# Kernel tuning notes

Measured on AMD Instinct MI355X. Metric: run time of the kernel, lower is better.

Reference implementation:

```python
import jax, jax.numpy as jnp
import numpy as np

BETA = 0.95
THRESH = 1.0
T = 25
MAXD = 11      # dilated_kernel_size: 250//25=10 -> bumped to odd 11
LP = 10        # left_pad = 250//25
B = 1024
SIGINIT = 5.0  # max_delay // 2, SIG is frozen at this value


@jax.custom_vjp
def atan_spike(u):
    # heaviside forward, atan surrogate gradient (snntorch surrogate.atan, alpha=2)
    return (u > 0).astype(u.dtype)

def _atan_fwd(u):
    return atan_spike(u), u

def _atan_bwd(u, g):
    return (g / (1.0 + (jnp.pi * u) ** 2),)

atan_spike.defvjp(_atan_fwd, _atan_bwd)


def dcls_kernel(W, P, SIG):
    # DCLS 'gauss': gaussian-interpolated dense kernel.
    # W: (O, I, kc), P/SIG: (1, O, I, kc) -> dense kernel (O, I, MAXD)
    idx = jnp.arange(MAXD, dtype=W.dtype)
    Pc = P[0] + MAXD // 2                      # center positions in dense kernel
    S = jnp.abs(SIG[0]) + 0.27                 # sigma floor (DCLS epsilon)
    X = jnp.exp(-0.5 * ((idx[:, None, None, None] - Pc) / S) ** 2)  # (K,O,I,kc)
    X = X / (X.sum(axis=0, keepdims=True) + 1e-7)
    return jnp.einsum('oic,joic->oij', W, X)


def dcls_conv(x, W, P, SIG, b):
    # x: (B, C_in, L) -> (B, C_out, L - MAXD + 1), VALID conv like padding=0
    k = dcls_kernel(W, P, SIG)
    y = jax.lax.conv_general_dilated(x, k, (1,), 'VALID',
                                     dimension_numbers=('NCH', 'OIH', 'NCH'))
    return y + b[None, :, None]


def batchnorm(x, gamma, beta, mean, var, eps=1e-5):
    # eval-mode BatchNorm1d over (B, C, L)
    inv = gamma / jnp.sqrt(var + eps)
    return (x - mean[None, :, None]) * inv[None, :, None] + beta[None, :, None]


def lif_scan(x):
    # snntorch Leaky, reset_mechanism='subtract'; x: (B, C, T) input currents
    xT = jnp.moveaxis(x, 2, 0)  # (T, B, C)

    def step(mem, xt):
        reset = jax.lax.stop_gradient(atan_spike(mem - THRESH))  # detached reset
        mem = BETA * mem + xt - reset * THRESH
        spk = atan_spike(mem - THRESH)
        return mem, (spk, mem)

    _, (spk, mem) = jax.lax.scan(step, jnp.zeros_like(xT[0]), xT)
    return spk, mem  # each (T, B, C)


def pad_left(x):
    return jnp.pad(x, ((0, 0), (0, 0), (LP, 0)))


def setup_inputs() -> dict:
    key = jax.random.key(0)
    ks = jax.random.split(key, 16)

    def w_init(k, o, i):
        return jax.random.normal(k, (o, i, 1), jnp.float32) / np.sqrt(i)

    inp = {
        'data': jax.random.normal(ks[0], (B, T, 140), jnp.float32),
        'W1': w_init(ks[1], 256, 140),
        'b1': jax.random.normal(ks[2], (256,), jnp.float32) * 0.01,
        'P1': jax.random.uniform(ks[3], (1, 256, 140, 1), jnp.float32, -SIGINIT, SIGINIT),
        'SIG1': jnp.full((1, 256, 140, 1), SIGINIT, jnp.float32),
        'bn1_gamma': jax.random.uniform(ks[4], (256,), jnp.float32, 0.5, 1.5),
        'bn1_beta': jax.random.normal(ks[5], (256,), jnp.float32) * 0.1,
        'bn1_mean': jax.random.normal(ks[6], (256,), jnp.float32) * 0.1,
        'bn1_var': jax.random.uniform(ks[7], (256,), jnp.float32, 0.5, 1.5),
        'W2': w_init(ks[8], 256, 256),
        'b2': jax.random.normal(ks[9], (256,), jnp.float32) * 0.01,
        'P2': jax.random.uniform(ks[10], (1, 256, 256, 1), jnp.float32, -SIGINIT, SIGINIT),
        'SIG2': jnp.full((1, 256, 256, 1), SIGINIT, jnp.float32),
        'bn2_gamma': jax.random.uniform(ks[11], (256,), jnp.float32, 0.5, 1.5),
        'bn2_beta': jax.random.normal(ks[12], (256,), jnp.float32) * 0.1,
        'bn2_mean': jax.random.normal(ks[13], (256,), jnp.float32) * 0.1,
        'bn2_var': jax.random.uniform(ks[14], (256,), jnp.float32, 0.5, 1.5),
        'W3': w_init(ks[15], 20, 256),
        'b3': jnp.zeros((20,), jnp.float32),
        'P3': jax.random.uniform(jax.random.fold_in(key, 99), (1, 20, 256, 1), jnp.float32, -SIGINIT, SIGINIT),
        'SIG3': jnp.full((1, 20, 256, 1), SIGINIT, jnp.float32),
    }
    return inp


def reference(data, W1, b1, P1, SIG1, bn1_gamma, bn1_beta, bn1_mean, bn1_var,
              W2, b2, P2, SIG2, bn2_gamma, bn2_beta, bn2_mean, bn2_var,
              W3, b3, P3, SIG3):
    # data: (B, T, 140); pad time dim on the left, then to (B, C, L)
    x = jnp.moveaxis(jnp.pad(data, ((0, 0), (LP, 0), (0, 0))), 1, 2)  # (B,140,T+LP)
    x = batchnorm(dcls_conv(x, W1, P1, SIG1, b1), bn1_gamma, bn1_beta, bn1_mean, bn1_var)
    spk1, _ = lif_scan(x)                  # (T, B, 256)
    in1 = jnp.moveaxis(spk1, 0, 2)         # (B, 256, T)  (dropout eval = identity)

    x = batchnorm(dcls_conv(pad_left(in1), W2, P2, SIG2, b2),
                  bn2_gamma, bn2_beta, bn2_mean, bn2_var)
    spk2, _ = lif_scan(x)
    in2 = jnp.moveaxis(spk2, 0, 2)         # (B, 256, T)

    x = dcls_conv(pad_left(in2), W3, P3, SIG3, b3)  # (B, 20, T)
    spk3, mem3 = lif_scan(x)               # (T, B, 20) each
    return spk3, mem3
```

## Files before the change

kernel.cpp:

```cpp
#include <hip/hip_runtime.h>
#include <math.h>

#define BB 1024
#define TT 25
#define LP 10
#define MAXD 11

#define XR2 26
#define XC 264
#define XSZ2 (XR2 * XC)

#define IC1 140
#define ICP1 160
#define XC1 168
#define XSZ1 (XR2 * XC1)
#define SS1 (2 * XSZ1)

typedef __bf16 bf16x8 __attribute__((ext_vector_type(8)));
typedef float  f32x4  __attribute__((ext_vector_type(4)));

#define MFMA16(A, B, C) __builtin_amdgcn_mfma_f32_16x16x32_bf16((A), (B), (C), 0, 0, 0)

__global__ void gen_trip(const float* __restrict__ W,
                         const float* __restrict__ P,
                         const float* __restrict__ SIG,
                         __bf16* __restrict__ Khi, __bf16* __restrict__ Kmid,
                         __bf16* __restrict__ Klo,
                         int O, int Opad, int I, int Ipad) {
    int idx = blockIdx.x * blockDim.x + threadIdx.x;
    if (idx >= Opad * Ipad) return;
    int i = idx % Ipad;
    int o = idx / Ipad;
    if (o >= O || i >= I) {
#pragma unroll
        for (int j = 0; j < MAXD; ++j) {
            size_t ofs = ((size_t)(j * Opad + o)) * Ipad + i;
            Khi[ofs] = (__bf16)0.0f;
            Kmid[ofs] = (__bf16)0.0f;
            Klo[ofs] = (__bf16)0.0f;
        }
        return;
    }
    int widx = o * I + i;
    float w  = W[widx];
    float pc = P[widx] + (float)(MAXD / 2);
    float s  = fabsf(SIG[widx]) + 0.27f;
    float x[MAXD];
    float sum = 0.f;
#pragma unroll
    for (int j = 0; j < MAXD; ++j) {
        float d = ((float)j - pc) / s;
        x[j] = expf(-0.5f * d * d);
        sum += x[j];
    }
    float denom = sum + 1e-7f;
#pragma unroll
    for (int j = 0; j < MAXD; ++j) {
        float kv = w * (x[j] / denom);
        __bf16 h = (__bf16)kv;
        float  r1 = kv - (float)h;
        __bf16 m = (__bf16)r1;
        float  r2 = r1 - (float)m;
        __bf16 l = (__bf16)r2;
        size_t ofs = ((size_t)(j * Opad + o)) * Ipad + i;
        Khi[ofs] = h;
        Kmid[ofs] = m;
        Klo[ofs] = l;
    }
}

__global__ __launch_bounds__(512, 2)
void conv1_mfma(const float* __restrict__ xin,
                const __bf16* __restrict__ Khi,
                const __bf16* __restrict__ Kmid,
                const __bf16* __restrict__ Klo,
                const float* __restrict__ bias,
                const float* __restrict__ gamma,
                const float* __restrict__ beta,
                const float* __restrict__ mean,
                const float* __restrict__ var,
                __bf16* __restrict__ spk1) {
    __shared__ __align__(16) char smem[3 * SS1 * 2];
    __bf16* xs = (__bf16*)smem;
    float*  ys = (float*)smem;

    const int rr = blockIdx.x & 7;
    const int gg = blockIdx.x >> 3;
    const int pp = 2 * (rr + 8 * (gg >> 1)) + (gg & 1);
    const int b0 = pp * 2;

    const int tid  = threadIdx.x;
    const int w    = tid >> 6;
    const int lane = tid & 63;
    const int lm   = lane & 15;
    const int quad = lane >> 4;

    {
        uint32_t* xz = (uint32_t*)smem;
        for (int k = tid; k < 3 * SS1 / 2; k += 512) xz[k] = 0u;
    }
    __syncthreads();
#pragma unroll
    for (int bl = 0; bl < 2; ++bl) {
        const float* src = xin + (size_t)(b0 + bl) * (TT * IC1);
        for (int k = tid; k < TT * IC1; k += 512) {
            int t = k / IC1;
            int i = k - t * IC1;
            float x  = src[k];
            __bf16 h = (__bf16)x;
            float r1 = x - (float)h;
            __bf16 m = (__bf16)r1;
            float r2 = r1 - (float)m;
            __bf16 l = (__bf16)r2;
            int ofs = bl * XSZ1 + t * XC1 + i;
            xs[0 * SS1 + ofs] = h;
            xs[1 * SS1 + ofs] = m;
            xs[2 * SS1 + ofs] = l;
        }
    }
    __syncthreads();

    f32x4 acc[2][4];
#pragma unroll
    for (int p = 0; p < 2; ++p)
#pragma unroll
        for (int nt = 0; nt < 4; ++nt) acc[p][nt] = (f32x4){0.f, 0.f, 0.f, 0.f};

    auto loadA = [&](int n, bf16x8* Ah, bf16x8* Am, bf16x8* Al) {
        n = (n > 54) ? 54 : n;
        const int j = n / 5;
        const int ic = n - 5 * j;
        const size_t base =
            (size_t)(j * 256 + w * 32 + lm) * ICP1 + ic * 32 + quad * 8;
#pragma unroll
        for (int p = 0; p < 2; ++p) {
            Ah[p] = *(const bf16x8*)(Khi  + base + p * 16 * ICP1);
            Am[p] = *(const bf16x8*)(Kmid + base + p * 16 * ICP1);
            Al[p] = *(const bf16x8*)(Klo  + base + p * 16 * ICP1);
        }
    };

    auto step = [&](int n, bf16x8* Ah, bf16x8* Am, bf16x8* Al) {
        const int j = n / 5;
        const int ic = n - 5 * j;
        int r0 = lm + j - 10;          r0 = ((unsigned)r0 < 25u) ? r0 : 25;
        int r1 = 16 + lm + j - 10;     r1 = ((unsigned)r1 < 25u) ? r1 : 25;
        const int col = ic * 32 + quad * 8;
#pragma unroll
        for (int bl = 0; bl < 2; ++bl) {
            bf16x8 Bh[2], Bm[2], Bl[2];
#pragma unroll
            for (int th = 0; th < 2; ++th) {
                const int row = th ? r1 : r0;
                const int ofs = bl * XSZ1 + row * XC1 + col;
                Bh[th] = *(const bf16x8*)&xs[0 * SS1 + ofs];
                Bm[th] = *(const bf16x8*)&xs[1 * SS1 + ofs];
                Bl[th] = *(const bf16x8*)&xs[2 * SS1 + ofs];
            }
#pragma unroll
            for (int p = 0; p < 2; ++p)
#pragma unroll
                for (int th = 0; th < 2; ++th)
                    acc[p][bl * 2 + th] = MFMA16(Ah[p], Bh[th], acc[p][bl * 2 + th]);
#pragma unroll
            for (int p = 0; p < 2; ++p)
#pragma unroll
                for (int th = 0; th < 2; ++th)
                    acc[p][bl * 2 + th] = MFMA16(Ah[p], Bm[th], acc[p][bl * 2 + th]);
#pragma unroll
            for (int p = 0; p < 2; ++p)
#pragma unroll
                for (int th = 0; th < 2; ++th)
                    acc[p][bl * 2 + th] = MFMA16(Am[p], Bh[th], acc[p][bl * 2 + th]);
#pragma unroll
            for (int p = 0; p < 2; ++p)
#pragma unroll
                for (int th = 0; th < 2; ++th)
                    acc[p][bl * 2 + th] = MFMA16(Ah[p], Bl[th], acc[p][bl * 2 + th]);
#pragma unroll
            for (int p = 0; p < 2; ++p)
#pragma unroll
                for (int th = 0; th < 2; ++th)
                    acc[p][bl * 2 + th] = MFMA16(Am[p], Bm[th], acc[p][bl * 2 + th]);
#pragma unroll
            for (int p = 0; p < 2; ++p)
#pragma unroll
                for (int th = 0; th < 2; ++th)
                    acc[p][bl * 2 + th] = MFMA16(Al[p], Bh[th], acc[p][bl * 2 + th]);
        }
    };

    bf16x8 A0h[2], A0m[2], A0l[2], A1h[2], A1m[2], A1l[2];
    loadA(0, A0h, A0m, A0l);
    for (int n = 0; n < 54; n += 2) {
        loadA(n + 1, A1h, A1m, A1l);
        step(n, A0h, A0m, A0l);
        loadA(n + 2, A0h, A0m, A0l);
        step(n + 1, A1h, A1m, A1l);
    }
    step(54, A0h, A0m, A0l);

#pragma unroll
    for (int bl = 0; bl < 2; ++bl) {
        __syncthreads();
#pragma unroll
        for (int p = 0; p < 2; ++p)
#pragma unroll
            for (int th = 0; th < 2; ++th) {
                int t = th * 16 + lm;
                if (t < TT) {
                    int ob = w * 32 + p * 16 + quad * 4;
#pragma unroll
                    for (int v = 0; v < 4; ++v)
                        ys[(ob + v) * 27 + t] = acc[p][bl * 2 + th][v];
                }
            }
        __syncthreads();
        if (tid < 256) {
            const int o = tid;
            float scale = gamma[o] / sqrtf(var[o] + 1e-5f);
            float ofs   = (bias[o] - mean[o]) * scale + beta[o];
            unsigned short* dst =
                (unsigned short*)spk1 + (size_t)(b0 + bl) * (TT * 256) + o;
            const float* yrow = &ys[o * 27];
            float memv = 0.f;
#pragma unroll
            for (int t = 0; t < TT; ++t) {
                float a     = yrow[t] * scale + ofs;
                float reset = (memv > 1.0f) ? 1.0f : 0.f;
                memv        = 0.95f * memv + a - reset;
                dst[t * 256] = (memv > 1.0f) ? 0x3F80 : 0;
            }
        }
    }
}

__attribute__((amdgpu_waves_per_eu(4, 4)))
__global__ __launch_bounds__(512)
void conv2_mfma(const __bf16* __restrict__ spk1,
                const __bf16* __restrict__ Khi,
                const __bf16* __restrict__ Kmid,
                const __bf16* __restrict__ Klo,
                const float* __restrict__ bias,
                const float* __restrict__ gamma,
                const float* __restrict__ beta,
                const float* __restrict__ mean,
                const float* __restrict__ var,
                __bf16* __restrict__ spk2) {
    __shared__ __align__(16) char smem[68224];
    __bf16* xs  = (__bf16*)smem;
    float*  ysq = (float*)(smem + 54912);

    const int h    = blockIdx.x & 1;
    const int bg   = blockIdx.x >> 1;
    const int b0   = bg * 4;
    const int oc0  = h * 128;

    const int tid  = threadIdx.x;
    const int w    = tid >> 6;
    const int wc   = w & 3;
    const int kg   = w >> 2;
    const int lane = tid & 63;
    const int lm   = lane & 15;
    const int quad = lane >> 4;

    for (int k = tid; k < 4 * (XC / 2); k += 512) {
        int bl = k / (XC / 2);
        int c  = k % (XC / 2);
        ((uint32_t*)xs)[(bl * XSZ2 + 25 * XC) / 2 + c] = 0u;
    }
    for (int k = tid; k < 4 * 800; k += 512) {
        int bl = k / 800;
        int v  = k % 800;
        int t  = v >> 5;
        int iv = v & 31;
        uint4 d = ((const uint4*)(spk1 + (size_t)(b0 + bl) * (TT * 256)))[v];
        *(uint4*)&xs[bl * XSZ2 + t * XC + iv * 8] = d;
    }
    __syncthreads();

    f32x4 acc[2][8];
#pragma unroll
    for (int pi = 0; pi < 2; ++pi)
#pragma unroll
        for (int nt = 0; nt < 8; ++nt) acc[pi][nt] = (f32x4){0.f, 0.f, 0.f, 0.f};

    {
        const int n0 = kg * 44;
#pragma unroll 1
        for (int n = n0; n < n0 + 44; ++n) {
            const int j = n >> 3, ic = n & 7;
            const size_t base =
                (size_t)(j * 256 + oc0 + wc * 32 + lm) * 256 + ic * 32 + quad * 8;
            bf16x8 Ah0 = *(const bf16x8*)(Khi  + base);
            bf16x8 Ah1 = *(const bf16x8*)(Khi  + base + 16 * 256);
            bf16x8 Am0 = *(const bf16x8*)(Kmid + base);
            bf16x8 Am1 = *(const bf16x8*)(Kmid + base + 16 * 256);
            bf16x8 Al0 = *(const bf16x8*)(Klo  + base);
            bf16x8 Al1 = *(const bf16x8*)(Klo  + base + 16 * 256);
            int r0 = lm + j - 10;          r0 = ((unsigned)r0 < 25u) ? r0 : 25;
            int r1 = 16 + lm + j - 10;     r1 = ((unsigned)r1 < 25u) ? r1 : 25;
            const int col = ic * 32 + quad * 8;
#pragma unroll
            for (int bl = 0; bl < 4; ++bl) {
                bf16x8 B0 = *(const bf16x8*)&xs[bl * XSZ2 + r0 * XC + col];
                bf16x8 B1 = *(const bf16x8*)&xs[bl * XSZ2 + r1 * XC + col];
                const int t0 = bl * 2, t1 = bl * 2 + 1;
                acc[0][t0] = MFMA16(Ah0, B0, acc[0][t0]);
                acc[1][t0] = MFMA16(Ah1, B0, acc[1][t0]);
                acc[0][t1] = MFMA16(Ah0, B1, acc[0][t1]);
                acc[1][t1] = MFMA16(Ah1, B1, acc[1][t1]);
                acc[0][t0] = MFMA16(Am0, B0, acc[0][t0]);
                acc[1][t0] = MFMA16(Am1, B0, acc[1][t0]);
                acc[0][t1] = MFMA16(Am0, B1, acc[0][t1]);
                acc[1][t1] = MFMA16(Am1, B1, acc[1][t1]);
                acc[0][t0] = MFMA16(Al0, B0, acc[0][t0]);
                acc[1][t0] = MFMA16(Al1, B0, acc[1][t0]);
                acc[0][t1] = MFMA16(Al0, B1, acc[0][t1]);
                acc[1][t1] = MFMA16(Al1, B1, acc[1][t1]);
            }
        }
    }

#pragma unroll
    for (int bl = 0; bl < 4; ++bl) {
#pragma unroll
        for (int q = 0; q < 2; ++q) {
            __syncthreads();
            if ((wc >> 1) == q) {
#pragma unroll
                for (int pi = 0; pi < 2; ++pi)
#pragma unroll
                    for (int th = 0; th < 2; ++th) {
                        int t = th * 16 + lm;
                        if (t < TT) {
                            int ol = (wc & 1) * 32 + pi * 16 + quad * 4;
#pragma unroll
                            for (int v = 0; v < 4; ++v)
                                ysq[(kg * 64 + ol + v) * 26 + t] =
                                    acc[pi][bl * 2 + th][v];
                        }
                    }
            }
            __syncthreads();
            if (tid < 64) {
                const int o = oc0 + q * 64 + tid;
                float scale = gamma[o] / sqrtf(var[o] + 1e-5f);
                float ofs   = (bias[o] - mean[o]) * scale + beta[o];
                const float* yr0 = &ysq[tid * 26];
                const float* yr1 = &ysq[(64 + tid) * 26];
                unsigned short* dst =
                    (unsigned short*)spk2 + (size_t)(b0 + bl) * (TT * 256) + o;
                float memv = 0.f;
#pragma unroll
                for (int t = 0; t < TT; ++t) {
                    float a     = (yr0[t] + yr1[t]) * scale + ofs;
                    float reset = (memv > 1.0f) ? 1.0f : 0.f;
                    memv        = 0.95f * memv + a - reset;
                    dst[t * 256] = (memv > 1.0f) ? 0x3F80 : 0;
                }
            }
        }
    }
}

__global__ __launch_bounds__(512, 2)
void conv3_mfma(const __bf16* __restrict__ spk2,
                const __bf16* __restrict__ K3hi,
                const __bf16* __restrict__ K3mid,
                const __bf16* __restrict__ K3lo,
                const float* __restrict__ b3,
                float* __restrict__ out) {
    __shared__ __align__(16) char smem[54912];
    __bf16* xs  = (__bf16*)smem;
    float*  ys3 = (float*)smem;

    const int b0   = blockIdx.x * 4;
    const int tid  = threadIdx.x;
    const int w    = tid >> 6;
    const int lane = tid & 63;
    const int lm   = lane & 15;
    const int quad = lane >> 4;

    for (int k = tid; k < 4 * (XC / 2); k += 512) {
        int bl = k / (XC / 2);
        int c  = k % (XC / 2);
        ((uint32_t*)xs)[(bl * XSZ2 + 25 * XC) / 2 + c] = 0u;
    }
    for (int k = tid; k < 4 * 800; k += 512) {
        int bl = k / 800;
        int v  = k % 800;
        int t  = v >> 5;
        int iv = v & 31;
        uint4 d = ((const uint4*)(spk2 + (size_t)(b0 + bl) * (TT * 256)))[v];
        *(uint4*)&xs[bl * XSZ2 + t * XC + iv * 8] = d;
    }
    __syncthreads();

    {
        const int p3  = w >> 2;
        const int bl3 = w & 3;
        f32x4 accH[2], accM[2], accL[2];
#pragma unroll
        for (int th = 0; th < 2; ++th) {
            accH[th] = (f32x4){0.f, 0.f, 0.f, 0.f};
            accM[th] = (f32x4){0.f, 0.f, 0.f, 0.f};
            accL[th] = (f32x4){0.f, 0.f, 0.f, 0.f};
        }

        auto loadA3 = [&](int n, bf16x8* Ah, bf16x8* Am, bf16x8* Al) {
            n = (n > 87) ? 87 : n;
            const int j = n >> 3, ic = n & 7;
            const size_t kofs =
                ((size_t)(j * 32 + p3 * 16 + lm)) * 256 + ic * 32 + quad * 8;
            *Ah = *(const bf16x8*)(K3hi  + kofs);
            *Am = *(const bf16x8*)(K3mid + kofs);
            *Al = *(const bf16x8*)(K3lo  + kofs);
        };
        auto step3 = [&](int n, bf16x8 Ah, bf16x8 Am, bf16x8 Al) {
            const int j = n >> 3, ic = n & 7;
#pragma unroll
            for (int th = 0; th < 2; ++th) {
                int r = th * 16 + lm + j - 10;
                r = ((unsigned)r < 25u) ? r : 25;
                bf16x8 Bf =
                    *(const bf16x8*)&xs[bl3 * XSZ2 + r * XC + ic * 32 + quad * 8];
                accH[th] = MFMA16(Ah, Bf, accH[th]);
                accM[th] = MFMA16(Am, Bf, accM[th]);
                accL[th] = MFMA16(Al, Bf, accL[th]);
            }
        };

        bf16x8 A0h, A0m, A0l, A1h, A1m, A1l;
        loadA3(0, &A0h, &A0m, &A0l);
        for (int n = 0; n < 86; n += 2) {
            loadA3(n + 1, &A1h, &A1m, &A1l);
            step3(n, A0h, A0m, A0l);
            loadA3(n + 2, &A0h, &A0m, &A0l);
            step3(n + 1, A1h, A1m, A1l);
        }
        loadA3(87, &A1h, &A1m, &A1l);
        step3(86, A0h, A0m, A0l);
        step3(87, A1h, A1m, A1l);

        __syncthreads();
#pragma unroll
        for (int th = 0; th < 2; ++th) {
            int t = th * 16 + lm;
            if (t < TT) {
#pragma unroll
                for (int v = 0; v < 4; ++v)
                    ys3[(bl3 * 32 + p3 * 16 + quad * 4 + v) * 26 + t] =
                        accH[th][v] + accM[th][v] + accL[th][v];
            }
        }
        __syncthreads();

        if (tid < 80) {
            const int bl2 = tid / 20;
            const int o   = tid % 20;
            float memv = 0.f;
            float bo   = b3[o];
            const float* yrow = &ys3[(bl2 * 32 + o) * 26];
#pragma unroll
            for (int t = 0; t < TT; ++t) {
                float a     = yrow[t] + bo;
                float reset = (memv > 1.0f) ? 1.0f : 0.f;
                memv        = 0.95f * memv + a - reset;
                float spk   = (memv > 1.0f) ? 1.0f : 0.f;
                out[(t * BB + (b0 + bl2)) * 20 + o]               = spk;
                out[TT * BB * 20 + (t * BB + (b0 + bl2)) * 20 + o] = memv;
            }
        }
    }
}

extern "C" void kernel_launch(void* const* d_in, const int* in_sizes, int n_in,
                              void* d_out, int out_size, void* d_ws, size_t ws_size,
                              hipStream_t stream) {
    const float* data = (const float*)d_in[0];
    const float* W1   = (const float*)d_in[1];
    const float* b1   = (const float*)d_in[2];
    const float* P1   = (const float*)d_in[3];
    const float* SIG1 = (const float*)d_in[4];
    const float* g1   = (const float*)d_in[5];
    const float* be1  = (const float*)d_in[6];
    const float* m1   = (const float*)d_in[7];
    const float* v1   = (const float*)d_in[8];
    const float* W2   = (const float*)d_in[9];
    const float* b2   = (const float*)d_in[10];
    const float* P2   = (const float*)d_in[11];
    const float* SIG2 = (const float*)d_in[12];
    const float* g2   = (const float*)d_in[13];
    const float* be2  = (const float*)d_in[14];
    const float* m2   = (const float*)d_in[15];
    const float* v2   = (const float*)d_in[16];
    const float* W3   = (const float*)d_in[17];
    const float* b3   = (const float*)d_in[18];
    const float* P3   = (const float*)d_in[19];
    const float* SIG3 = (const float*)d_in[20];
    float* out = (float*)d_out;

    char* p = (char*)d_ws;
    __bf16* K1hi  = (__bf16*)p;  p += 901120;
    __bf16* K1mid = (__bf16*)p;  p += 901120;
    __bf16* K1lo  = (__bf16*)p;  p += 901120;
    __bf16* spk1  = (__bf16*)p;  p += 13107200;
    __bf16* K2hi  = (__bf16*)p;  p += 1441792;
    __bf16* K2mid = (__bf16*)p;  p += 1441792;
    __bf16* K2lo  = (__bf16*)p;  p += 1441792;
    __bf16* K3hi  = (__bf16*)p;  p += 180224;
    __bf16* K3mid = (__bf16*)p;  p += 180224;
    __bf16* K3lo  = (__bf16*)p;  p += 180224;
    __bf16* spk2  = (__bf16*)p;

    gen_trip<<<(256 * 160 + 255) / 256, 256, 0, stream>>>(
        W1, P1, SIG1, K1hi, K1mid, K1lo, 256, 256, 140, 160);
    gen_trip<<<(256 * 256 + 255) / 256, 256, 0, stream>>>(
        W2, P2, SIG2, K2hi, K2mid, K2lo, 256, 256, 256, 256);
    gen_trip<<<(32 * 256 + 255) / 256, 256, 0, stream>>>(
        W3, P3, SIG3, K3hi, K3mid, K3lo, 20, 32, 256, 256);

    conv1_mfma<<<BB / 2, 512, 0, stream>>>(data, K1hi, K1mid, K1lo,
                                           b1, g1, be1, m1, v1, spk1);
    conv2_mfma<<<BB / 2, 512, 0, stream>>>(spk1, K2hi, K2mid, K2lo,
                                           b2, g2, be2, m2, v2, spk2);
    conv3_mfma<<<BB / 4, 512, 0, stream>>>(spk2, K3hi, K3mid, K3lo, b3, out);
}
```

Measured before the change: 417.0 us.

## Process eight batch rows per conv2 block and double-buffer kernel weight loads

conv2 now handles 8 batch items per block instead of 4, so each weight fragment loaded from global memory feeds twice as many MFMAs. The grid is halved and shared memory nearly doubles. Weight loads are also software-pipelined with two register buffers so the next tap's fragments load while the current tap computes. The cost is a 32-entry accumulator set and more registers, which is why occupancy is forced down to 2 waves per EU.

```diff
diff --git a/kernel.cpp b/kernel.cpp
--- a/kernel.cpp
+++ b/kernel.cpp
@@ -235,7 +235,7 @@
     }
 }
 
-__attribute__((amdgpu_waves_per_eu(4, 4)))
+__attribute__((amdgpu_waves_per_eu(2, 2)))
 __global__ __launch_bounds__(512)
 void conv2_mfma(const __bf16* __restrict__ spk1,
                 const __bf16* __restrict__ Khi,
@@ -247,13 +247,13 @@
                 const float* __restrict__ mean,
                 const float* __restrict__ var,
                 __bf16* __restrict__ spk2) {
-    __shared__ __align__(16) char smem[68224];
+    __shared__ __align__(16) char smem[123136];
     __bf16* xs  = (__bf16*)smem;
-    float*  ysq = (float*)(smem + 54912);
+    float*  ysq = (float*)(smem + 109824);
 
     const int h    = blockIdx.x & 1;
     const int bg   = blockIdx.x >> 1;
-    const int b0   = bg * 4;
+    const int b0   = bg * 8;
     const int oc0  = h * 128;
 
     const int tid  = threadIdx.x;
@@ -264,12 +264,12 @@
     const int lm   = lane & 15;
     const int quad = lane >> 4;
 
-    for (int k = tid; k < 4 * (XC / 2); k += 512) {
+    for (int k = tid; k < 8 * (XC / 2); k += 512) {
         int bl = k / (XC / 2);
         int c  = k % (XC / 2);
         ((uint32_t*)xs)[(bl * XSZ2 + 25 * XC) / 2 + c] = 0u;
     }
-    for (int k = tid; k < 4 * 800; k += 512) {
+    for (int k = tid; k < 8 * 800; k += 512) {
         int bl = k / 800;
         int v  = k % 800;
         int t  = v >> 5;
@@ -279,51 +279,68 @@
     }
     __syncthreads();
 
-    f32x4 acc[2][8];
+    f32x4 acc[2][16];
 #pragma unroll
     for (int pi = 0; pi < 2; ++pi)
 #pragma unroll
-        for (int nt = 0; nt < 8; ++nt) acc[pi][nt] = (f32x4){0.f, 0.f, 0.f, 0.f};
+        for (int nt = 0; nt < 16; ++nt) acc[pi][nt] = (f32x4){0.f, 0.f, 0.f, 0.f};
 
     {
         const int n0 = kg * 44;
-#pragma unroll 1
-        for (int n = n0; n < n0 + 44; ++n) {
+        auto loadA = [&](int n, bf16x8* A) {
             const int j = n >> 3, ic = n & 7;
             const size_t base =
                 (size_t)(j * 256 + oc0 + wc * 32 + lm) * 256 + ic * 32 + quad * 8;
-            bf16x8 Ah0 = *(const bf16x8*)(Khi  + base);
-            bf16x8 Ah1 = *(const bf16x8*)(Khi  + base + 16 * 256);
-            bf16x8 Am0 = *(const bf16x8*)(Kmid + base);
-            bf16x8 Am1 = *(const bf16x8*)(Kmid + base + 16 * 256);
-            bf16x8 Al0 = *(const bf16x8*)(Klo  + base);
-            bf16x8 Al1 = *(const bf16x8*)(Klo  + base + 16 * 256);
+            A[0] = *(const bf16x8*)(Khi  + base);
+            A[1] = *(const bf16x8*)(Khi  + base + 16 * 256);
+            A[2] = *(const bf16x8*)(Kmid + base);
+            A[3] = *(const bf16x8*)(Kmid + base + 16 * 256);
+            A[4] = *(const bf16x8*)(Klo  + base);
+            A[5] = *(const bf16x8*)(Klo  + base + 16 * 256);
+        };
+        auto step = [&](int n, const bf16x8* A) {
+            const int j = n >> 3, ic = n & 7;
             int r0 = lm + j - 10;          r0 = ((unsigned)r0 < 25u) ? r0 : 25;
             int r1 = 16 + lm + j - 10;     r1 = ((unsigned)r1 < 25u) ? r1 : 25;
             const int col = ic * 32 + quad * 8;
 #pragma unroll
-            for (int bl = 0; bl < 4; ++bl) {
-                bf16x8 B0 = *(const bf16x8*)&xs[bl * XSZ2 + r0 * XC + col];
-                bf16x8 B1 = *(const bf16x8*)&xs[bl * XSZ2 + r1 * XC + col];
-                const int t0 = bl * 2, t1 = bl * 2 + 1;
-                acc[0][t0] = MFMA16(Ah0, B0, acc[0][t0]);
-                acc[1][t0] = MFMA16(Ah1, B0, acc[1][t0]);
-                acc[0][t1] = MFMA16(Ah0, B1, acc[0][t1]);
-                acc[1][t1] = MFMA16(Ah1, B1, acc[1][t1]);
-                acc[0][t0] = MFMA16(Am0, B0, acc[0][t0]);
-                acc[1][t0] = MFMA16(Am1, B0, acc[1][t0]);
-                acc[0][t1] = MFMA16(Am0, B1, acc[0][t1]);
-                acc[1][t1] = MFMA16(Am1, B1, acc[1][t1]);
-                acc[0][t0] = MFMA16(Al0, B0, acc[0][t0]);
-                acc[1][t0] = MFMA16(Al1, B0, acc[1][t0]);
-                acc[0][t1] = MFMA16(Al0, B1, acc[0][t1]);
-                acc[1][t1] = MFMA16(Al1, B1, acc[1][t1]);
-            }
-        }
-    }
-
-#pragma unroll
-    for (int bl = 0; bl < 4; ++bl) {
+            for (int bp = 0; bp < 4; ++bp) {
+                const int blA = bp * 2, blB = bp * 2 + 1;
+                bf16x8 B0A = *(const bf16x8*)&xs[blA * XSZ2 + r0 * XC + col];
+                bf16x8 B1A = *(const bf16x8*)&xs[blA * XSZ2 + r1 * XC + col];
+                bf16x8 B0B = *(const bf16x8*)&xs[blB * XSZ2 + r0 * XC + col];
+                bf16x8 B1B = *(const bf16x8*)&xs[blB * XSZ2 + r1 * XC + col];
+                const int a0 = blA * 2, a1 = blA * 2 + 1;
+                const int a2 = blB * 2, a3 = blB * 2 + 1;
+#pragma unroll
+                for (int s = 0; s < 3; ++s) {
+                    acc[0][a0] = MFMA16(A[s * 2 + 0], B0A, acc[0][a0]);
+                    acc[1][a0] = MFMA16(A[s * 2 + 1], B0A, acc[1][a0]);
+                    acc[0][a1] = MFMA16(A[s * 2 + 0], B1A, acc[0][a1]);
+                    acc[1][a1] = MFMA16(A[s * 2 + 1], B1A, acc[1][a1]);
+                    acc[0][a2] = MFMA16(A[s * 2 + 0], B0B, acc[0][a2]);
+                    acc[1][a2] = MFMA16(A[s * 2 + 1], B0B, acc[1][a2]);
+                    acc[0][a3] = MFMA16(A[s * 2 + 0], B1B, acc[0][a3]);
+                    acc[1][a3] = MFMA16(A[s * 2 + 1], B1B, acc[1][a3]);
+                }
+            }
+        };
+
+        bf16x8 A0[6], A1[6];
+        loadA(n0, A0);
+        for (int n = n0; n < n0 + 42; n += 2) {
+            loadA(n + 1, A1);
+            step(n, A0);
+            loadA(n + 2, A0);
+            step(n + 1, A1);
+        }
+        loadA(n0 + 43, A1);
+        step(n0 + 42, A0);
+        step(n0 + 43, A1);
+    }
+
+#pragma unroll
+    for (int bl = 0; bl < 8; ++bl) {
 #pragma unroll
         for (int q = 0; q < 2; ++q) {
             __syncthreads();
@@ -523,7 +540,7 @@
 
     conv1_mfma<<<BB / 2, 512, 0, stream>>>(data, K1hi, K1mid, K1lo,
                                            b1, g1, be1, m1, v1, spk1);
-    conv2_mfma<<<BB / 2, 512, 0, stream>>>(spk1, K2hi, K2mid, K2lo,
+    conv2_mfma<<<BB / 4, 512, 0, stream>>>(spk1, K2hi, K2mid, K2lo,
                                            b2, g2, be2, m2, v2, spk2);
     conv3_mfma<<<BB / 4, 512, 0, stream>>>(spk2, K3hi, K3mid, K3lo, b3, out);
 }
```

Result: faster. 401.0 us (-3.8%).
